# Kernel tuning notes

Measured on AMD Instinct MI355X. Metric: run time of the kernel, lower is better.

## Reference

```python
import jax, jax.numpy as jnp
import numpy as np

THRESH = 0.1        # spike_threshold
GRAD_WIDTH = 1.0    # width_grad
GRAD_SCALE = 1.0    # scale_grad

# SingleSpike with SingleExponential surrogate gradient (sinabs/EXODUS semantics)
@jax.custom_vjp
def single_spike(v):
    return (v >= THRESH).astype(v.dtype)

def _spk_fwd(v):
    return single_spike(v), v

def _spk_bwd(v, g):
    abs_width = GRAD_WIDTH * THRESH
    surr = (GRAD_SCALE / abs_width) * jnp.exp(-jnp.abs(v - THRESH) / abs_width)
    return (g * surr,)

single_spike.defvjp(_spk_fwd, _spk_bwd)

def weight_norm(v, g):
    # torch weight_norm: w = g * v / ||v|| with norm over all dims except dim 0
    norm = jnp.sqrt(jnp.sum(v * v, axis=tuple(range(1, v.ndim)), keepdims=True))
    return g.reshape((-1,) + (1,) * (v.ndim - 1)) * v / norm

def conv2d_same(x, w):
    return jax.lax.conv_general_dilated(
        x, w, window_strides=(1, 1), padding='SAME',
        dimension_numbers=('NCHW', 'OIHW', 'NCHW'))

def avg_pool2(x):
    s = jax.lax.reduce_window(x, 0.0, jax.lax.add, (1, 1, 2, 2), (1, 1, 2, 2), 'VALID')
    return s * 0.25

def iaf_squeeze(syn, batch_size):
    # syn: (B*T, C, H, W); IAFSqueeze: unflatten time, integrate-and-fire recurrence,
    # single spike per step, membrane-subtract reset, re-flatten.
    bt = syn.shape[0]
    t = bt // batch_size
    syn = syn.reshape(batch_size, t, *syn.shape[1:])
    def step(v, inp):
        v = v + inp
        s = single_spike(v)
        return v - THRESH * s, s
    v0 = jnp.zeros_like(syn[:, 0])
    _, spikes = jax.lax.scan(step, v0, jnp.moveaxis(syn, 1, 0))  # (T, B, C, H, W)
    out = jnp.moveaxis(spikes, 0, 1)
    return out.reshape(bt, *out.shape[2:])

def _forward(x, conv_params, lin_v, lin_g):
    b, t = x.shape[0], x.shape[1]
    h = x.reshape(b * t, *x.shape[2:])  # flatten(0,1)
    for v, g in conv_params:
        h = iaf_squeeze(conv2d_same(h, weight_norm(v, g)), b)
        if h.shape[-1] > 4:
            h = avg_pool2(h)
    w = weight_norm(lin_v, lin_g)           # (11, C*4*4)
    out = h.reshape(b * t, -1) @ w.T        # (B*T, 11)
    return out.reshape(b, t, out.shape[-1])

def setup_inputs() -> dict:
    key = jax.random.key(0)
    ks = jax.random.split(key, 6)
    B, T, H = 32, 50, 64
    chans = [2, 8, 16, 32, 64]
    d = {'x': jax.random.uniform(ks[0], (B, T, 2, H, H), dtype=jnp.float32)}
    for i in range(4):
        d[f'conv{i}_v'] = jax.random.normal(ks[1 + i], (chans[i + 1], chans[i], 3, 3), jnp.float32)
        d[f'conv{i}_g'] = jnp.ones((chans[i + 1],), jnp.float32)
    d['lin_v'] = jax.random.normal(ks[5], (11, 64 * 4 * 4), jnp.float32)
    d['lin_g'] = jnp.ones((11,), jnp.float32)
    return d

def reference(x, conv0_v, conv0_g, conv1_v, conv1_g, conv2_v, conv2_g, conv3_v, conv3_g, lin_v, lin_g):
    conv_params = [(conv0_v, conv0_g), (conv1_v, conv1_g), (conv2_v, conv2_g), (conv3_v, conv3_g)]
    return _forward(x, conv_params, lin_v, lin_g)
```

## Files before the change

kernel.cpp:

```cpp
#include <hip/hip_runtime.h>

#define THRESH 0.1f

typedef float    f4 __attribute__((ext_vector_type(4)));
typedef float    f2 __attribute__((ext_vector_type(2)));
typedef _Float16 h8 __attribute__((ext_vector_type(8)));
typedef _Float16 h4 __attribute__((ext_vector_type(4)));
typedef _Float16 h2 __attribute__((ext_vector_type(2)));

__global__ void wnorm_all(const float* __restrict__ c0v, const float* __restrict__ c0g,
                          const float* __restrict__ c1v, const float* __restrict__ c1g,
                          const float* __restrict__ c2v, const float* __restrict__ c2g,
                          const float* __restrict__ c3v, const float* __restrict__ c3g,
                          const float* __restrict__ lv,  const float* __restrict__ lg,
                          float* __restrict__ w0, float* __restrict__ w1,
                          float* __restrict__ w2, float* __restrict__ w3,
                          float* __restrict__ wl) {
    int rb = blockIdx.x;
    const float *v, *g; float* w; int fanin, row;
    if (rb < 8)        { v = c0v; g = c0g; w = w0; fanin = 18;   row = rb; }
    else if (rb < 24)  { v = c1v; g = c1g; w = w1; fanin = 72;   row = rb - 8; }
    else if (rb < 56)  { v = c2v; g = c2g; w = w2; fanin = 144;  row = rb - 24; }
    else if (rb < 120) { v = c3v; g = c3g; w = w3; fanin = 288;  row = rb - 56; }
    else               { v = lv;  g = lg;  w = wl; fanin = 1024; row = rb - 120; }
    const bool perm = (rb >= 120);

    const float* vr = v + (size_t)row * fanin;
    float ss = 0.f;
    for (int i = threadIdx.x; i < fanin; i += 64) { float x = vr[i]; ss = fmaf(x, x, ss); }
    #pragma unroll
    for (int off = 32; off > 0; off >>= 1) ss += __shfl_down(ss, off);
    ss = __shfl(ss, 0);
    float scale = g[row] / sqrtf(ss);
    float* wr = w + (size_t)row * fanin;
    for (int i = threadIdx.x; i < fanin; i += 64) {
        int d = perm ? (((i & 15) << 6) | (i >> 4)) : i;
        wr[d] = vr[i] * scale;
    }
}

template<int CIN, int H, int COUT, int CG, int WX, int SEGS, int BDIM, int PSB>
__launch_bounds__(BDIM)
__global__ void conv_iaf_pool(const void* __restrict__ in_, const float* __restrict__ w,
                              _Float16* __restrict__ out, int B, int T) {
    constexpr bool HIN  = (CIN % 8 == 0);
    constexpr int Hp    = H / 2;
    constexpr int PP    = Hp * Hp;
    constexpr int HH    = H * H;
    constexpr int WY    = 64 / WX;
    constexpr int NW    = BDIM / 64;
    constexpr int NWps  = NW / SEGS;
    constexpr int XW    = H / WX;
    constexpr int YWV   = NWps / XW;
    constexpr int RPB   = YWV * WY;
    constexpr int STRIPS= H / RPB;
    constexpr int CGRP  = COUT / (CG * SEGS);
    constexpr int SR    = RPB + 2;
    constexpr int COLS  = H + 2;
    constexpr int SLABB = SR * COLS * PSB;
    constexpr bool FULLY= (RPB == H);
    constexpr int R0    = FULLY ? 1 : 0;
    constexpr int NR    = FULLY ? H : SR;
    constexpr int UPC   = HIN ? (CIN / 8) : 1;
    constexpr int NU    = NR * H * UPC;
    constexpr int ITERS = (NU + BDIM - 1) / BDIM;
    constexpr bool GUARD= !(FULLY && (NU % BDIM == 0));

    __shared__ alignas(16) char slab[2][SLABB];

    const int tid = threadIdx.x;
    const int G = gridDim.x, bx = blockIdx.x;
    const int pb = (bx & 7) * (G >> 3) + (bx >> 3);
    const int cgb   = pb % CGRP;
    const int strip = (pb / CGRP) % STRIPS;
    const int b     = pb / (CGRP * STRIPS);

    const int wid = tid >> 6, l = tid & 63;
    const int seg = wid / NWps;
    const int wlv = wid % NWps;
    const int xw = wlv % XW, yw = wlv / XW;
    const int xl = l % WX, ylw = l / WX;
    const int x  = xw * WX + xl;
    const int yy = yw * WY + ylw;
    const int y0 = strip * RPB;
    const int y  = y0 + yy;

    const int c0 = __builtin_amdgcn_readfirstlane((cgb * SEGS + seg) * CG);
    const float* __restrict__ wu = w + (size_t)c0 * (CIN * 9);

    int addrB[9];
    #pragma unroll
    for (int dr = 0; dr < 3; ++dr)
        #pragma unroll
        for (int dc = 0; dc < 3; ++dc)
            addrB[dr * 3 + dc] = ((yy + dr) * COLS + (x + dc)) * PSB;

    int goff[ITERS], loffB[ITERS];
    #pragma unroll
    for (int i = 0; i < ITERS; ++i) {
        const int idx = tid + i * BDIM;
        int j, gx, rr0;
        if constexpr (HIN) { j = idx % UPC; gx = (idx / UPC) % H; rr0 = idx / (UPC * H); }
        else               { j = 0;         gx = idx % H;         rr0 = (idx / H) % NR; }
        const int rr = R0 + rr0;
        const int gy = y0 - 1 + rr;
        const bool ok = (idx < NU) && ((unsigned)gy < (unsigned)H);
        if constexpr (HIN) goff[i] = ok ? ((gy * H + gx) * UPC + j) : -1;
        else               goff[i] = ok ? (gy * H + gx) : -1;
        loffB[i] = ok ? ((rr * COLS + (gx + 1)) * PSB + 16 * j) : -1;
    }

    constexpr bool WREG = !HIN && (CG * CIN * 9) <= 80;
    float wreg[WREG ? (CG * CIN * 9) : 1];
    if constexpr (WREG) {
        #pragma unroll
        for (int i = 0; i < CG * CIN * 9; ++i) wreg[i] = wu[i];
    }

    for (int i = tid; i < (2 * SLABB) / 4; i += BDIM) ((int*)slab)[i] = 0;
    __syncthreads();

    float vmem[CG];
    #pragma unroll
    for (int c = 0; c < CG; ++c) vmem[c] = 0.f;

    f4 pf[ITERS];
    #define GATHER(t_)                                                            \
        if constexpr (HIN) {                                                      \
            const f4* inb = (const f4*)in_ + (size_t)(b * T + (t_)) * (HH * UPC); \
            _Pragma("unroll")                                                     \
            for (int i = 0; i < ITERS; ++i) {                                     \
                f4 r_ = {0.f, 0.f, 0.f, 0.f};                                     \
                if (!GUARD || goff[i] >= 0) r_ = inb[goff[i]];                    \
                pf[i] = r_;                                                       \
            }                                                                     \
        } else {                                                                  \
            const float* inb = (const float*)in_ + (size_t)(b * T + (t_)) * (CIN * HH); \
            _Pragma("unroll")                                                     \
            for (int i = 0; i < ITERS; ++i) {                                     \
                f4 r_ = {0.f, 0.f, 0.f, 0.f};                                     \
                if (goff[i] >= 0) { r_.x = inb[goff[i]]; r_.y = inb[goff[i] + HH]; } \
                pf[i] = r_;                                                       \
            }                                                                     \
        }
    #define STAGE(buf)                                                            \
        _Pragma("unroll")                                                         \
        for (int i = 0; i < ITERS; ++i) {                                         \
            if (!GUARD || loffB[i] >= 0) {                                        \
                if constexpr (HIN) *(f4*)(&slab[buf][loffB[i]]) = pf[i];          \
                else { f2 v2_; v2_.x = pf[i].x; v2_.y = pf[i].y;                  \
                       *(f2*)(&slab[buf][loffB[i]]) = v2_; }                      \
            }                                                                     \
        }

    {
        GATHER(0)
        STAGE(0)
        GATHER(1)
    }
    __syncthreads();

    for (int t = 0; t < T; ++t) {
        if (t + 1 < T) { STAGE((t + 1) & 1) }
        if (t + 2 < T) { GATHER(t + 2) }

        const char* sb = slab[t & 1];
        float acc[CG];
        #pragma unroll
        for (int c = 0; c < CG; ++c) acc[c] = 0.f;

        if constexpr (HIN) {
            #pragma unroll
            for (int o = 0; o < CIN / 8; ++o) {
                h8 P[9];
                #pragma unroll
                for (int k = 0; k < 9; ++k)
                    P[k] = *(const h8*)(sb + addrB[k] + 16 * o);
                #pragma unroll
                for (int cid = 0; cid < 8; ++cid) {
                    const int ci = 8 * o + cid;
                    #pragma unroll
                    for (int c = 0; c < CG; ++c)
                        #pragma unroll
                        for (int k = 0; k < 9; ++k)
                            acc[c] = fmaf((float)P[k][cid],
                                          wu[(size_t)(c * CIN + ci) * 9 + k], acc[c]);
                }
            }
        } else {
            f2 P[9];
            #pragma unroll
            for (int k = 0; k < 9; ++k)
                P[k] = *(const f2*)(sb + addrB[k]);
            #pragma unroll
            for (int cid = 0; cid < 2; ++cid)
                #pragma unroll
                for (int c = 0; c < CG; ++c)
                    #pragma unroll
                    for (int k = 0; k < 9; ++k)
                        acc[c] = fmaf(P[k][cid],
                                      WREG ? wreg[(c * CIN + cid) * 9 + k]
                                           : wu[(size_t)(c * CIN + cid) * 9 + k],
                                      acc[c]);
        }

        float sv[CG];
        #pragma unroll
        for (int c = 0; c < CG; ++c) {
            vmem[c] += acc[c];
            float s = (vmem[c] >= THRESH) ? 1.f : 0.f;
            vmem[c] -= THRESH * s;
            float sum = s;
            sum += __shfl_xor(sum, 1);
            sum += __shfl_xor(sum, WX);
            sv[c] = 0.25f * sum;
        }
        if (((xl | ylw) & 1) == 0) {
            const size_t ob = ((size_t)(b * T + t) * PP + (y >> 1) * Hp + (x >> 1)) * COUT + c0;
            if constexpr (CG == 4) {
                h4 hv = {(_Float16)sv[0], (_Float16)sv[1], (_Float16)sv[2], (_Float16)sv[3]};
                *(h4*)(out + ob) = hv;
            } else if constexpr (CG == 2) {
                h2 hv = {(_Float16)sv[0], (_Float16)sv[1]};
                *(h2*)(out + ob) = hv;
            } else {
                out[ob] = (_Float16)sv[0];
            }
        }
        __syncthreads();
    }
    #undef GATHER
    #undef STAGE
}

__global__ void linear_kernel(const _Float16* __restrict__ h, const float* __restrict__ w,
                              float* __restrict__ out) {
    __shared__ float hs[1024];
    __shared__ float part[16][17];
    const int n = blockIdx.x;
    for (int i = threadIdx.x; i < 1024; i += blockDim.x)
        hs[i] = (float)h[(size_t)n * 1024 + i];
    __syncthreads();
    const int j = threadIdx.x & 15, ch = threadIdx.x >> 4;
    float acc = 0.f;
    if (j < 11) {
        const float* wr = w + (size_t)j * 1024 + ch * 64;
        const float* hh = hs + ch * 64;
        #pragma unroll 8
        for (int k = 0; k < 64; ++k) acc = fmaf(hh[k], wr[k], acc);
    }
    part[j][ch] = acc;
    __syncthreads();
    if (threadIdx.x < 11) {
        float s = 0.f;
        #pragma unroll
        for (int cc = 0; cc < 16; ++cc) s += part[threadIdx.x][cc];
        out[(size_t)n * 11 + threadIdx.x] = s;
    }
}

extern "C" void kernel_launch(void* const* d_in, const int* in_sizes, int n_in,
                              void* d_out, int out_size, void* d_ws, size_t ws_size,
                              hipStream_t stream) {
    const int B = 32, T = 50;

    const float* x   = (const float*)d_in[0];
    const float* c0v = (const float*)d_in[1];
    const float* c0g = (const float*)d_in[2];
    const float* c1v = (const float*)d_in[3];
    const float* c1g = (const float*)d_in[4];
    const float* c2v = (const float*)d_in[5];
    const float* c2g = (const float*)d_in[6];
    const float* c3v = (const float*)d_in[7];
    const float* c3g = (const float*)d_in[8];
    const float* lv  = (const float*)d_in[9];
    const float* lg  = (const float*)d_in[10];
    float* out = (float*)d_out;

    float* ws = (float*)d_ws;
    float* w0 = ws;
    float* w1 = w0 + 144;
    float* w2 = w1 + 1152;
    float* w3 = w2 + 4608;
    float* wl = w3 + 18432;
    _Float16* bufA16 = (_Float16*)(ws + 40960);
    _Float16* bufB16 = (_Float16*)(ws + 40960 + 13107200);

    wnorm_all<<<131, 64, 0, stream>>>(c0v, c0g, c1v, c1g, c2v, c2g, c3v, c3g,
                                      lv, lg, w0, w1, w2, w3, wl);

    conv_iaf_pool<2,  64, 8,  4, 32, 1, 256, 8 ><<<1024, 256, 0, stream>>>(x,       w0, bufA16, B, T);
    conv_iaf_pool<8,  32, 16, 4, 32, 1, 256, 16><<<512,  256, 0, stream>>>(bufA16,  w1, bufB16, B, T);
    conv_iaf_pool<16, 16, 32, 2, 16, 2, 256, 48><<<512,  256, 0, stream>>>(bufB16,  w2, bufA16, B, T);
    conv_iaf_pool<32, 8,  64, 1, 8,  4, 256, 80><<<512,  256, 0, stream>>>(bufA16,  w3, bufB16, B, T);

    linear_kernel<<<B * T, 256, 0, stream>>>(bufB16, wl, out);
}
```

Measured before the change: 551.5 us.

## Process two timesteps per iteration to reuse weights in conv layers 2-3

Adds a TP template parameter so the conv+IAF kernel can stage two timesteps into shared memory and compute both convolutions in one pass. Each weight load then feeds FMAs for both timesteps, and one barrier covers two steps. Layers 2 and 3 switch to this mode with new channel-group, segment, block and grid shapes. The cost is more registers and shared memory per block and fewer blocks for layer 2, which may reduce occupancy.

```diff
diff --git a/kernel.cpp b/kernel.cpp
--- a/kernel.cpp
+++ b/kernel.cpp
@@ -39,7 +39,7 @@
     }
 }
 
-template<int CIN, int H, int COUT, int CG, int WX, int SEGS, int BDIM, int PSB>
+template<int CIN, int H, int COUT, int CG, int WX, int SEGS, int BDIM, int PSB, int TP>
 __launch_bounds__(BDIM)
 __global__ void conv_iaf_pool(const void* __restrict__ in_, const float* __restrict__ w,
                               _Float16* __restrict__ out, int B, int T) {
@@ -66,7 +66,7 @@
     constexpr int ITERS = (NU + BDIM - 1) / BDIM;
     constexpr bool GUARD= !(FULLY && (NU % BDIM == 0));
 
-    __shared__ alignas(16) char slab[2][SLABB];
+    __shared__ alignas(16) char slab[2 * TP][SLABB];
 
     const int tid = threadIdx.x;
     const int G = gridDim.x, bx = blockIdx.x;
@@ -117,22 +117,22 @@
         for (int i = 0; i < CG * CIN * 9; ++i) wreg[i] = wu[i];
     }
 
-    for (int i = tid; i < (2 * SLABB) / 4; i += BDIM) ((int*)slab)[i] = 0;
+    for (int i = tid; i < (2 * TP * SLABB) / 4; i += BDIM) ((int*)slab)[i] = 0;
     __syncthreads();
 
     float vmem[CG];
     #pragma unroll
     for (int c = 0; c < CG; ++c) vmem[c] = 0.f;
 
-    f4 pf[ITERS];
-    #define GATHER(t_)                                                            \
+    f4 pf[TP][ITERS];
+    #define GATHER(ph, t_)                                                        \
         if constexpr (HIN) {                                                      \
             const f4* inb = (const f4*)in_ + (size_t)(b * T + (t_)) * (HH * UPC); \
             _Pragma("unroll")                                                     \
             for (int i = 0; i < ITERS; ++i) {                                     \
                 f4 r_ = {0.f, 0.f, 0.f, 0.f};                                     \
                 if (!GUARD || goff[i] >= 0) r_ = inb[goff[i]];                    \
-                pf[i] = r_;                                                       \
+                pf[ph][i] = r_;                                                   \
             }                                                                     \
         } else {                                                                  \
             const float* inb = (const float*)in_ + (size_t)(b * T + (t_)) * (CIN * HH); \
@@ -140,35 +140,22 @@
             for (int i = 0; i < ITERS; ++i) {                                     \
                 f4 r_ = {0.f, 0.f, 0.f, 0.f};                                     \
                 if (goff[i] >= 0) { r_.x = inb[goff[i]]; r_.y = inb[goff[i] + HH]; } \
-                pf[i] = r_;                                                       \
+                pf[ph][i] = r_;                                                   \
             }                                                                     \
         }
-    #define STAGE(buf)                                                            \
+    #define STAGE(buf, ph)                                                        \
         _Pragma("unroll")                                                         \
         for (int i = 0; i < ITERS; ++i) {                                         \
             if (!GUARD || loffB[i] >= 0) {                                        \
-                if constexpr (HIN) *(f4*)(&slab[buf][loffB[i]]) = pf[i];          \
-                else { f2 v2_; v2_.x = pf[i].x; v2_.y = pf[i].y;                  \
+                if constexpr (HIN) *(f4*)(&slab[buf][loffB[i]]) = pf[ph][i];      \
+                else { f2 v2_; v2_.x = pf[ph][i].x; v2_.y = pf[ph][i].y;          \
                        *(f2*)(&slab[buf][loffB[i]]) = v2_; }                      \
             }                                                                     \
         }
 
-    {
-        GATHER(0)
-        STAGE(0)
-        GATHER(1)
-    }
-    __syncthreads();
-
-    for (int t = 0; t < T; ++t) {
-        if (t + 1 < T) { STAGE((t + 1) & 1) }
-        if (t + 2 < T) { GATHER(t + 2) }
-
-        const char* sb = slab[t & 1];
-        float acc[CG];
+    auto conv1 = [&](const char* sb, float* acc) {
         #pragma unroll
         for (int c = 0; c < CG; ++c) acc[c] = 0.f;
-
         if constexpr (HIN) {
             #pragma unroll
             for (int o = 0; o < CIN / 8; ++o) {
@@ -203,7 +190,37 @@
                                            : wu[(size_t)(c * CIN + cid) * 9 + k],
                                       acc[c]);
         }
-
+    };
+
+    auto conv2 = [&](const char* sbA, const char* sbB, float* accA, float* accB) {
+        #pragma unroll
+        for (int c = 0; c < CG; ++c) { accA[c] = 0.f; accB[c] = 0.f; }
+        if constexpr (HIN) {
+            #pragma unroll
+            for (int o = 0; o < CIN / 8; ++o) {
+                h8 PA[9], PB[9];
+                #pragma unroll
+                for (int k = 0; k < 9; ++k) {
+                    PA[k] = *(const h8*)(sbA + addrB[k] + 16 * o);
+                    PB[k] = *(const h8*)(sbB + addrB[k] + 16 * o);
+                }
+                #pragma unroll
+                for (int cid = 0; cid < 8; ++cid) {
+                    const int ci = 8 * o + cid;
+                    #pragma unroll
+                    for (int c = 0; c < CG; ++c)
+                        #pragma unroll
+                        for (int k = 0; k < 9; ++k) {
+                            const float wv = wu[(size_t)(c * CIN + ci) * 9 + k];
+                            accA[c] = fmaf((float)PA[k][cid], wv, accA[c]);
+                            accB[c] = fmaf((float)PB[k][cid], wv, accB[c]);
+                        }
+                }
+            }
+        }
+    };
+
+    auto fire = [&](float* acc, int t_) {
         float sv[CG];
         #pragma unroll
         for (int c = 0; c < CG; ++c) {
@@ -216,7 +233,7 @@
             sv[c] = 0.25f * sum;
         }
         if (((xl | ylw) & 1) == 0) {
-            const size_t ob = ((size_t)(b * T + t) * PP + (y >> 1) * Hp + (x >> 1)) * COUT + c0;
+            const size_t ob = ((size_t)(b * T + t_) * PP + (y >> 1) * Hp + (x >> 1)) * COUT + c0;
             if constexpr (CG == 4) {
                 h4 hv = {(_Float16)sv[0], (_Float16)sv[1], (_Float16)sv[2], (_Float16)sv[3]};
                 *(h4*)(out + ob) = hv;
@@ -227,7 +244,43 @@
                 out[ob] = (_Float16)sv[0];
             }
         }
+    };
+
+    if constexpr (TP == 1) {
+        {
+            GATHER(0, 0)
+            STAGE(0, 0)
+            GATHER(0, 1)
+        }
         __syncthreads();
+        for (int t = 0; t < T; ++t) {
+            if (t + 1 < T) { STAGE((t + 1) & 1, 0) }
+            if (t + 2 < T) { GATHER(0, t + 2) }
+            float acc[CG];
+            conv1(slab[t & 1], acc);
+            fire(acc, t);
+            __syncthreads();
+        }
+    } else {
+        {
+            GATHER(0, 0)
+            GATHER(1, 1)
+            STAGE(0, 0)
+            STAGE(1, 1)
+            GATHER(0, 2)
+            GATHER(1, 3)
+        }
+        __syncthreads();
+        for (int tt = 0; tt < T; tt += 2) {
+            const int p = (tt >> 1) & 1;
+            if (tt + 2 < T) { STAGE(2 * (p ^ 1), 0) STAGE(2 * (p ^ 1) + 1, 1) }
+            if (tt + 4 < T) { GATHER(0, tt + 4) GATHER(1, tt + 5) }
+            float accA[CG], accB[CG];
+            conv2(&slab[2 * p][0], &slab[2 * p + 1][0], accA, accB);
+            fire(accA, tt);
+            fire(accB, tt + 1);
+            __syncthreads();
+        }
     }
     #undef GATHER
     #undef STAGE
@@ -289,10 +342,10 @@
     wnorm_all<<<131, 64, 0, stream>>>(c0v, c0g, c1v, c1g, c2v, c2g, c3v, c3g,
                                       lv, lg, w0, w1, w2, w3, wl);
 
-    conv_iaf_pool<2,  64, 8,  4, 32, 1, 256, 8 ><<<1024, 256, 0, stream>>>(x,       w0, bufA16, B, T);
-    conv_iaf_pool<8,  32, 16, 4, 32, 1, 256, 16><<<512,  256, 0, stream>>>(bufA16,  w1, bufB16, B, T);
-    conv_iaf_pool<16, 16, 32, 2, 16, 2, 256, 48><<<512,  256, 0, stream>>>(bufB16,  w2, bufA16, B, T);
-    conv_iaf_pool<32, 8,  64, 1, 8,  4, 256, 80><<<512,  256, 0, stream>>>(bufA16,  w3, bufB16, B, T);
+    conv_iaf_pool<2,  64, 8,  4, 32, 1, 256, 8 , 1><<<1024, 256, 0, stream>>>(x,       w0, bufA16, B, T);
+    conv_iaf_pool<8,  32, 16, 4, 32, 1, 256, 16, 1><<<512,  256, 0, stream>>>(bufA16,  w1, bufB16, B, T);
+    conv_iaf_pool<16, 16, 32, 4, 16, 1, 256, 48, 2><<<256,  256, 0, stream>>>(bufB16,  w2, bufA16, B, T);
+    conv_iaf_pool<32, 8,  64, 2, 8,  2, 128, 80, 2><<<512,  128, 0, stream>>>(bufA16,  w3, bufB16, B, T);
 
     linear_kernel<<<B * T, 256, 0, stream>>>(bufB16, wl, out);
 }
```

After: 716.4 us. 1.3x slower.
